# Performance work log

Measured on AMD Instinct MI355X. Metric: run time of the kernel, lower is better.

## Reference

```python
import jax, jax.numpy as jnp
import numpy as np

N, M, K = 100000, 50000, 8   # num vertices, num hyperedges, fixed hyperedge size
DIN, DOUT = 128, 128

def setup_inputs() -> dict:
    key = jax.random.key(0)
    k1, k2, k3 = jax.random.split(key, 3)
    X = jax.random.normal(k1, (N, DIN), jnp.float32)
    vertex = jax.random.randint(k2, (M * K,), 0, N)          # member vertices, flattened
    edges = jnp.repeat(jnp.arange(M), K)                     # hyperedge id per entry (sorted)
    W = jax.random.normal(k3, (DIN, DOUT), jnp.float32) / np.sqrt(DIN)
    b = jnp.zeros((DOUT,), jnp.float32)
    return {"X": X, "vertex": vertex, "edges": edges, "W": W, "b": b}

def reference(X, vertex, edges, W, b):
    # theta: Linear(in, out) applied BEFORE graph construction (as in dhg.HyperGCNConv)
    Y = X @ W + b                              # [N, DOUT]
    verts = vertex.reshape(M, K)               # hyperedge membership (edges = repeat(arange(M), K))
    feats = Y[verts]                           # [M, K, DOUT] gather
    # pairwise squared distances within each hyperedge
    sq = jnp.sum(feats * feats, axis=-1)                      # [M, K]
    d2 = sq[:, :, None] + sq[:, None, :] - 2.0 * jnp.einsum('mkd,mld->mkl', feats, feats)
    flat = jnp.argmax(d2.reshape(M, K * K), axis=1)
    ui, vi = flat // K, flat % K                              # argmax-distance pair positions
    u = jnp.take_along_axis(verts, ui[:, None], 1)[:, 0]      # [M]
    v = jnp.take_along_axis(verts, vi[:, None], 1)[:, 0]      # [M]
    w = jnp.float32(1.0 / (2 * K - 3))                        # HyperGCN mediator weight
    pos = jnp.arange(K)
    med = ((pos[None, :] != ui[:, None]) & (pos[None, :] != vi[:, None])).astype(Y.dtype)  # [M,K]
    # graph edges: (u,v) + (u,m),(v,m) for each mediator m; masked entries get weight 0
    src = jnp.concatenate([u, jnp.repeat(u, K), jnp.repeat(v, K)])
    dst = jnp.concatenate([v, verts.reshape(-1), verts.reshape(-1)])
    wts = jnp.concatenate([jnp.full((M,), w, Y.dtype), (med * w).reshape(-1), (med * w).reshape(-1)])
    # GCN smoothing: D^{-1/2} (A + I) D^{-1/2} Y with symmetric A, duplicate edges summed
    deg = jnp.ones((N,), Y.dtype).at[src].add(wts).at[dst].add(wts)
    dinv = jax.lax.rsqrt(deg)
    Xs = Y * dinv[:, None]
    out = Xs                                                  # self-loop term
    out = out.at[dst].add(wts[:, None] * Xs[src])
    out = out.at[src].add(wts[:, None] * Xs[dst])
    out = out * dinv[:, None]
    return jax.nn.relu(out)                                   # is_last=False -> ReLU (dropout=0)
```

## Files before the change

kernel.cpp:

```cpp
#include <hip/hip_runtime.h>
#include <hip/hip_bf16.h>

#define NV 100000
#define ME 50000
#define NINC (ME * 8)
#define NBLK ((NV + 255) / 256)
#define NRBG ((NV + 127) / 128)
constexpr float WMED = 1.0f / 13.0f;

typedef __attribute__((ext_vector_type(8))) short bf16x8;
typedef __attribute__((ext_vector_type(4))) float f32x4;

static __device__ inline void cvt_split8(const float4& a, const float4& b,
                                         bf16x8& hi, bf16x8& lo) {
    const float v[8] = {a.x, a.y, a.z, a.w, b.x, b.y, b.z, b.w};
    #pragma unroll
    for (int j = 0; j < 8; ++j) {
        __hip_bfloat16 h = __float2bfloat16(v[j]);
        const float hf = __bfloat162float(h);
        __hip_bfloat16 l = __float2bfloat16(v[j] - hf);
        union { __hip_bfloat16 b; short s; } uh{h}, ul{l};
        hi[j] = uh.s;
        lo[j] = ul.s;
    }
}

__global__ __launch_bounds__(256) void k_wsplit(const float* __restrict__ W,
                                                short* __restrict__ Wg) {
    const int idx = blockIdx.x * 256 + threadIdx.x;
    const int k = idx >> 7;
    const int c = idx & 127;
    const float w = W[idx];
    __hip_bfloat16 h = __float2bfloat16(w);
    const float hf = __bfloat162float(h);
    __hip_bfloat16 l = __float2bfloat16(w - hf);
    const int cb = c >> 6, gp = (c >> 4) & 3, m = c & 15;
    const int s = k >> 5, qq = (k >> 3) & 3, j = k & 7;
    const int base = cb * 1024 + (s * 4 + gp) * 64 + qq * 16 + m;
    union { __hip_bfloat16 b; short s; } uh{h}, ul{l};
    Wg[(long)base * 8 + j] = uh.s;
    Wg[(long)(2048 + base) * 8 + j] = ul.s;
}

__global__ __launch_bounds__(256, 4) void k_gemm(const float* __restrict__ X,
                                                 const uint4* __restrict__ Wg,
                                                 const float* __restrict__ bias,
                                                 float* __restrict__ Y,
                                                 __hip_bfloat16* __restrict__ Ybf) {
    const int t = threadIdx.x;
    const int wv = t >> 6;
    const int L  = t & 63;
    const int m  = L & 15;
    const int q  = L >> 4;

    const int rb = blockIdx.x >> 1;
    const int cb = blockIdx.x & 1;

    const int row_base = rb * 128 + wv * 32;
    int r0 = row_base + m;      if (r0 > NV - 1) r0 = NV - 1;
    int r1 = row_base + 16 + m; if (r1 > NV - 1) r1 = NV - 1;
    const float* p0 = X + (long)r0 * 128 + q * 8;
    const float* p1 = X + (long)r1 * 128 + q * 8;

    const bf16x8* Whf = (const bf16x8*)Wg + cb * 1024;
    const bf16x8* Wlf = (const bf16x8*)Wg + 2048 + cb * 1024;

    f32x4 acc[2][4];
    #pragma unroll
    for (int tt = 0; tt < 2; ++tt)
        #pragma unroll
        for (int g = 0; g < 4; ++g)
            acc[tt][g] = (f32x4){0.f, 0.f, 0.f, 0.f};

    float4 Ac0 = *(const float4*)(p0);
    float4 Ac1 = *(const float4*)(p0 + 4);
    float4 Ac2 = *(const float4*)(p1);
    float4 Ac3 = *(const float4*)(p1 + 4);

    #pragma unroll
    for (int s = 0; s < 4; ++s) {
        float4 An0, An1, An2, An3;
        if (s < 3) {
            An0 = *(const float4*)(p0 + (s + 1) * 32);
            An1 = *(const float4*)(p0 + (s + 1) * 32 + 4);
            An2 = *(const float4*)(p1 + (s + 1) * 32);
            An3 = *(const float4*)(p1 + (s + 1) * 32 + 4);
        }
        bf16x8 ah0, al0, ah1, al1;
        cvt_split8(Ac0, Ac1, ah0, al0);
        cvt_split8(Ac2, Ac3, ah1, al1);
        #pragma unroll
        for (int g = 0; g < 4; ++g) {
            const bf16x8 bh = Whf[(s * 4 + g) * 64 + L];
            const bf16x8 bl = Wlf[(s * 4 + g) * 64 + L];
            acc[0][g] = __builtin_amdgcn_mfma_f32_16x16x32_bf16(ah0, bh, acc[0][g], 0, 0, 0);
            acc[0][g] = __builtin_amdgcn_mfma_f32_16x16x32_bf16(ah0, bl, acc[0][g], 0, 0, 0);
            acc[0][g] = __builtin_amdgcn_mfma_f32_16x16x32_bf16(al0, bh, acc[0][g], 0, 0, 0);
            acc[1][g] = __builtin_amdgcn_mfma_f32_16x16x32_bf16(ah1, bh, acc[1][g], 0, 0, 0);
            acc[1][g] = __builtin_amdgcn_mfma_f32_16x16x32_bf16(ah1, bl, acc[1][g], 0, 0, 0);
            acc[1][g] = __builtin_amdgcn_mfma_f32_16x16x32_bf16(al1, bh, acc[1][g], 0, 0, 0);
        }
        if (s < 3) { Ac0 = An0; Ac1 = An1; Ac2 = An2; Ac3 = An3; }
    }

    float bc[4];
    #pragma unroll
    for (int g = 0; g < 4; ++g) bc[g] = bias[cb * 64 + g * 16 + m];

    #pragma unroll
    for (int tt = 0; tt < 2; ++tt) {
        #pragma unroll
        for (int r = 0; r < 4; ++r) {
            const int row = row_base + tt * 16 + q * 4 + r;
            float vg[4], vn[4];
            #pragma unroll
            for (int g = 0; g < 4; ++g) {
                vg[g] = acc[tt][g][r] + bc[g];
                vn[g] = __shfl_xor(vg[g], 1);
            }
            if (row < NV) {
                #pragma unroll
                for (int g = 0; g < 4; ++g)
                    Y[(long)row * 128 + cb * 64 + g * 16 + m] = vg[g];
                if ((L & 1) == 0) {
                    #pragma unroll
                    for (int g = 0; g < 4; ++g) {
                        __hip_bfloat162 h2;
                        h2.x = __float2bfloat16(vg[g]);
                        h2.y = __float2bfloat16(vn[g]);
                        *(__hip_bfloat162*)(Ybf + (long)row * 128 + cb * 64 + g * 16 + m) = h2;
                    }
                }
            }
        }
    }
}

__global__ __launch_bounds__(256) void k_edge(const float* __restrict__ Y,
                                              const int* __restrict__ vertex,
                                              int* __restrict__ uvpos) {
    const int wid = threadIdx.x >> 6;
    const int lane = threadIdx.x & 63;
    const int m = blockIdx.x * 4 + wid;

    const int x = lane & 15;
    const int q = lane >> 4;
    const int vr = vertex[m * 8 + (x & 7)];
    const float* rp = Y + (long)vr * 128 + q * 8;

    float4 A0[4], A1[4];
    #pragma unroll
    for (int s = 0; s < 4; ++s) {
        A0[s] = *(const float4*)(rp + s * 32);
        A1[s] = *(const float4*)(rp + s * 32 + 4);
    }

    f32x4 acc = (f32x4){0.f, 0.f, 0.f, 0.f};
    #pragma unroll
    for (int s = 0; s < 4; ++s) {
        bf16x8 ah, al;
        cvt_split8(A0[s], A1[s], ah, al);
        acc = __builtin_amdgcn_mfma_f32_16x16x32_bf16(ah, ah, acc, 0, 0, 0);
        acc = __builtin_amdgcn_mfma_f32_16x16x32_bf16(ah, al, acc, 0, 0, 0);
        acc = __builtin_amdgcn_mfma_f32_16x16x32_bf16(al, ah, acc, 0, 0, 0);
    }

    const int k = lane >> 3, l = lane & 7;
    const int srcG = l + 16 * (k >> 2);
    const int srcK = k + 16 * (k >> 2);
    const int srcL = l + 16 * (l >> 2);
    float g = 0.f, sk = 0.f, sl = 0.f;
    #pragma unroll
    for (int r = 0; r < 4; ++r) {
        const float tg = __shfl(acc[r], srcG);
        const float tk = __shfl(acc[r], srcK);
        const float tl = __shfl(acc[r], srcL);
        if ((k & 3) == r) { g = tg; sk = tk; }
        if ((l & 3) == r) sl = tl;
    }
    float v = sk + sl - 2.0f * g;

    int idx = lane;
    #pragma unroll
    for (int off = 32; off >= 1; off >>= 1) {
        const float ov = __shfl_xor(v, off);
        const int oi = __shfl_xor(idx, off);
        if (ov > v || (ov == v && oi < idx)) { v = ov; idx = oi; }
    }
    if (lane == 0) uvpos[m] = idx;
}

__global__ __launch_bounds__(256) void k_init(int* __restrict__ cnt,
                                              int* __restrict__ rowptr) {
    const int i = blockIdx.x * 256 + threadIdx.x;
    if (i < NV) cnt[i] = 0;
    if (i == 0) rowptr[NV] = NINC;
}

__global__ __launch_bounds__(256) void k_hist(const int* __restrict__ vertex,
                                              int* __restrict__ cnt) {
    const int j = blockIdx.x * 256 + threadIdx.x;
    if (j < NINC) atomicAdd(cnt + vertex[j], 1);
}

__global__ __launch_bounds__(256) void k_scan1(const int* __restrict__ cnt,
                                               int* __restrict__ bsum) {
    __shared__ int s[256];
    const int t = threadIdx.x;
    const int i = blockIdx.x * 256 + t;
    s[t] = (i < NV) ? cnt[i] : 0;
    __syncthreads();
    #pragma unroll
    for (int off = 128; off >= 1; off >>= 1) {
        if (t < off) s[t] += s[t + off];
        __syncthreads();
    }
    if (t == 0) bsum[blockIdx.x] = s[0];
}

__global__ __launch_bounds__(64) void k_scan2(const int* __restrict__ bsum,
                                              int* __restrict__ boff) {
    const int lane = threadIdx.x;
    int running = 0;
    for (int c = 0; c * 64 < NBLK; ++c) {
        const int idx = c * 64 + lane;
        int v = (idx < NBLK) ? bsum[idx] : 0;
        int x = v;
        #pragma unroll
        for (int off = 1; off < 64; off <<= 1) {
            const int n = __shfl_up(x, off);
            if (lane >= off) x += n;
        }
        if (idx < NBLK) boff[idx] = running + x - v;
        running += __shfl(x, 63);
    }
}

__global__ __launch_bounds__(256) void k_scan3(const int* __restrict__ cnt,
                                               const int* __restrict__ boff,
                                               int* __restrict__ rowptr,
                                               int* __restrict__ fill) {
    __shared__ int s[256];
    const int t = threadIdx.x;
    const int i = blockIdx.x * 256 + t;
    const int v = (i < NV) ? cnt[i] : 0;
    s[t] = v;
    __syncthreads();
    #pragma unroll
    for (int off = 1; off < 256; off <<= 1) {
        const int add = (t >= off) ? s[t - off] : 0;
        __syncthreads();
        s[t] += add;
        __syncthreads();
    }
    if (i < NV) {
        const int excl = boff[blockIdx.x] + s[t] - v;
        rowptr[i] = excl;
        fill[i] = excl;
    }
}

__global__ __launch_bounds__(256) void k_fill(const int* __restrict__ vertex,
                                              const int* __restrict__ uvpos,
                                              int* __restrict__ fill,
                                              int* __restrict__ entries) {
    const int j = blockIdx.x * 256 + threadIdx.x;
    if (j < NINC) {
        const int v = vertex[j];
        const int m = j >> 3, p = j & 7;
        const int idx = uvpos[m];
        const int role = (p == (idx >> 3) || p == (idx & 7)) ? 0 : 1;
        const int slot = atomicAdd(fill + v, 1);
        entries[slot] = (m << 1) | role;
    }
}

__global__ __launch_bounds__(256) void k_deg(const int* __restrict__ rowptr,
                                             const int* __restrict__ entries,
                                             float* __restrict__ deg) {
    const int i = blockIdx.x * 256 + threadIdx.x;
    if (i >= NV) return;
    const int start = rowptr[i], end = rowptr[i + 1];
    float d = 1.0f;
    for (int e = start; e < end; ++e)
        d += (entries[e] & 1) ? (2.0f * WMED) : (7.0f * WMED);
    deg[i] = d;
}

__global__ __launch_bounds__(256) void k_sp(const __hip_bfloat16* __restrict__ Ybf,
                                            const int* __restrict__ vertex,
                                            const int* __restrict__ uvpos,
                                            const float* __restrict__ deg,
                                            __hip_bfloat162* __restrict__ SP) {
    const int wid = threadIdx.x >> 6;
    const int lane = threadIdx.x & 63;
    const int m = blockIdx.x * 4 + wid;

    const int idx = uvpos[m];
    const int ui = idx >> 3, vi = idx & 7;

    float S0 = 0.f, S1 = 0.f, U0 = 0.f, U1 = 0.f, V0 = 0.f, V1 = 0.f;
    #pragma unroll
    for (int p = 0; p < 8; ++p) {
        const int vp = vertex[m * 8 + p];
        const float di = rsqrtf(deg[vp]);
        const __hip_bfloat162 y2 =
            ((const __hip_bfloat162*)(Ybf + (long)vp * 128))[lane];
        const float r0 = __bfloat162float(y2.x) * di;
        const float r1 = __bfloat162float(y2.y) * di;
        S0 += r0; S1 += r1;
        if (p == ui) { U0 = r0; U1 = r1; }
        if (p == vi) { V0 = r0; V1 = r1; }
    }
    __hip_bfloat162 s2, p2;
    s2.x = __float2bfloat16(WMED * S0);
    s2.y = __float2bfloat16(WMED * S1);
    p2.x = __float2bfloat16(WMED * (U0 + V0));
    p2.y = __float2bfloat16(WMED * (U1 + V1));
    SP[(long)(2 * m) * 64 + lane] = s2;
    SP[(long)(2 * m + 1) * 64 + lane] = p2;
}

__global__ __launch_bounds__(256) void k_gather(const float* __restrict__ Y,
                                                const float* __restrict__ deg,
                                                const int* __restrict__ rowptr,
                                                const int* __restrict__ entries,
                                                const __hip_bfloat162* __restrict__ SP,
                                                float* __restrict__ out) {
    const int wid = threadIdx.x >> 6;
    const int lane = threadIdx.x & 63;
    const int i = blockIdx.x * 4 + wid;

    const int start = rowptr[i], end = rowptr[i + 1];
    const int degc = end - start;
    const int tl = (lane < degc) ? entries[start + lane] : 0;

    const float din = rsqrtf(deg[i]);
    const float2 y = *(const float2*)(Y + (long)i * 128 + lane * 2);
    const float xs0 = y.x * din;
    const float xs1 = y.y * din;

    float a0 = 0.f, a1 = 0.f;
    float fnuv = 0.f;
    const int dmain = (degc < 64) ? degc : 64;

    for (int e = 0; e < dmain; e += 4) {
        const int j1 = (e + 1 < dmain) ? e + 1 : e;
        const int j2 = (e + 2 < dmain) ? e + 2 : e;
        const int j3 = (e + 3 < dmain) ? e + 3 : e;
        const float m1 = (e + 1 < dmain) ? 1.f : 0.f;
        const float m2 = (e + 2 < dmain) ? 1.f : 0.f;
        const float m3 = (e + 3 < dmain) ? 1.f : 0.f;
        const int t0 = __shfl(tl, e);
        const int t1 = __shfl(tl, j1);
        const int t2 = __shfl(tl, j2);
        const int t3 = __shfl(tl, j3);
        const __hip_bfloat162 T0 = SP[(long)t0 * 64 + lane];
        const __hip_bfloat162 T1 = SP[(long)t1 * 64 + lane];
        const __hip_bfloat162 T2 = SP[(long)t2 * 64 + lane];
        const __hip_bfloat162 T3 = SP[(long)t3 * 64 + lane];
        fnuv += (float)((t0 & 1) ^ 1) + m1 * (float)((t1 & 1) ^ 1)
              + m2 * (float)((t2 & 1) ^ 1) + m3 * (float)((t3 & 1) ^ 1);
        a0 += __bfloat162float(T0.x) + m1 * __bfloat162float(T1.x)
            + m2 * __bfloat162float(T2.x) + m3 * __bfloat162float(T3.x);
        a1 += __bfloat162float(T0.y) + m1 * __bfloat162float(T1.y)
            + m2 * __bfloat162float(T2.y) + m3 * __bfloat162float(T3.y);
    }
    for (int e2 = start + 64; e2 < end; ++e2) {
        const int t = entries[e2];
        const __hip_bfloat162 T = SP[(long)t * 64 + lane];
        fnuv += (float)((t & 1) ^ 1);
        a0 += __bfloat162float(T.x);
        a1 += __bfloat162float(T.y);
    }

    const float self = 1.0f - WMED * fnuv;
    a0 = fmaf(self, xs0, a0);
    a1 = fmaf(self, xs1, a1);
    float2 o;
    o.x = fmaxf(a0 * din, 0.0f);
    o.y = fmaxf(a1 * din, 0.0f);
    *(float2*)(out + (long)i * 128 + lane * 2) = o;
}

extern "C" void kernel_launch(void* const* d_in, const int* in_sizes, int n_in,
                              void* d_out, int out_size, void* d_ws, size_t ws_size,
                              hipStream_t stream) {
    const float* X      = (const float*)d_in[0];
    const int*   vertex = (const int*)d_in[1];
    const float* W      = (const float*)d_in[3];
    const float* bias   = (const float*)d_in[4];
    float* out = (float*)d_out;

    float* Y              = (float*)d_ws;
    __hip_bfloat16* Ybf   = (__hip_bfloat16*)(Y + (long)NV * 128);
    __hip_bfloat162* SP   = (__hip_bfloat162*)(Ybf + (long)NV * 128);
    float* deg            = (float*)((__hip_bfloat16*)SP + (long)2 * ME * 128);
    int*   uvpos          = (int*)(deg + NV);
    int*   cnt            = uvpos + ME;
    int*   rowptr         = cnt + NV;
    int*   fill           = rowptr + NV + 1;
    int*   bsum           = fill + NV;
    int*   boff           = bsum + NBLK;
    int*   entries        = boff + NBLK;
    char*  pW             = (char*)(entries + NINC);
    uint4* Wg             = (uint4*)(((uintptr_t)pW + 15) & ~(uintptr_t)15);

    k_wsplit<<<64, 256, 0, stream>>>(W, (short*)Wg);
    k_gemm <<<NRBG * 2, 256, 0, stream>>>(X, Wg, bias, Y, Ybf);
    k_edge <<<ME / 4, 256, 0, stream>>>(Y, vertex, uvpos);
    k_init <<<NBLK, 256, 0, stream>>>(cnt, rowptr);
    k_hist <<<(NINC + 255) / 256, 256, 0, stream>>>(vertex, cnt);
    k_scan1<<<NBLK, 256, 0, stream>>>(cnt, bsum);
    k_scan2<<<1, 64, 0, stream>>>(bsum, boff);
    k_scan3<<<NBLK, 256, 0, stream>>>(cnt, boff, rowptr, fill);
    k_fill <<<(NINC + 255) / 256, 256, 0, stream>>>(vertex, uvpos, fill, entries);
    k_deg  <<<NBLK, 256, 0, stream>>>(rowptr, entries, deg);
    k_sp   <<<ME / 4, 256, 0, stream>>>(Ybf, vertex, uvpos, deg, SP);
    k_gather<<<NV / 4, 256, 0, stream>>>(Y, deg, rowptr, entries, SP, out);
}
```

Baseline: 284.4 us.

## Compute edge distances with FP32 LDS dot products and fold degree into fill

The per-hyperedge pairwise distance kernel now stages the 8 member rows in shared memory and computes the 8x8 Gram matrix with FP32 FMAs, one pair per lane. This replaces the split-bf16 MFMA path and its shuffle gymnastics, and gives exact FP32 argmax. Separately, the degree computation kernel is removed: k_init sets deg to 1, and k_fill atomically adds each incidence's weight. This saves one launch and a CSR pass, at the cost of float atomics and a non-deterministic summation order.

```diff
diff --git a/kernel.cpp b/kernel.cpp
--- a/kernel.cpp
+++ b/kernel.cpp
@@ -139,47 +139,47 @@
 __global__ __launch_bounds__(256) void k_edge(const float* __restrict__ Y,
                                               const int* __restrict__ vertex,
                                               int* __restrict__ uvpos) {
+    __shared__ float sF[4][8 * 132];
     const int wid = threadIdx.x >> 6;
     const int lane = threadIdx.x & 63;
     const int m = blockIdx.x * 4 + wid;
-
-    const int x = lane & 15;
-    const int q = lane >> 4;
-    const int vr = vertex[m * 8 + (x & 7)];
-    const float* rp = Y + (long)vr * 128 + q * 8;
-
-    float4 A0[4], A1[4];
-    #pragma unroll
-    for (int s = 0; s < 4; ++s) {
-        A0[s] = *(const float4*)(rp + s * 32);
-        A1[s] = *(const float4*)(rp + s * 32 + 4);
-    }
-
-    f32x4 acc = (f32x4){0.f, 0.f, 0.f, 0.f};
-    #pragma unroll
-    for (int s = 0; s < 4; ++s) {
-        bf16x8 ah, al;
-        cvt_split8(A0[s], A1[s], ah, al);
-        acc = __builtin_amdgcn_mfma_f32_16x16x32_bf16(ah, ah, acc, 0, 0, 0);
-        acc = __builtin_amdgcn_mfma_f32_16x16x32_bf16(ah, al, acc, 0, 0, 0);
-        acc = __builtin_amdgcn_mfma_f32_16x16x32_bf16(al, ah, acc, 0, 0, 0);
-    }
+    float* F = sF[wid];
+
+    int verts[8];
+    #pragma unroll
+    for (int p = 0; p < 8; ++p) verts[p] = vertex[m * 8 + p];
+
+    #pragma unroll
+    for (int p = 0; p < 8; ++p) {
+        const float2 v = *(const float2*)(Y + (long)verts[p] * 128 + lane * 2);
+        *(float2*)(F + p * 132 + lane * 2) = v;
+    }
+    __syncthreads();
 
     const int k = lane >> 3, l = lane & 7;
-    const int srcG = l + 16 * (k >> 2);
-    const int srcK = k + 16 * (k >> 2);
-    const int srcL = l + 16 * (l >> 2);
-    float g = 0.f, sk = 0.f, sl = 0.f;
-    #pragma unroll
-    for (int r = 0; r < 4; ++r) {
-        const float tg = __shfl(acc[r], srcG);
-        const float tk = __shfl(acc[r], srcK);
-        const float tl = __shfl(acc[r], srcL);
-        if ((k & 3) == r) { g = tg; sk = tk; }
-        if ((l & 3) == r) sl = tl;
-    }
-    float v = sk + sl - 2.0f * g;
-
+    float a0 = 0.f, a1 = 0.f, a2 = 0.f, a3 = 0.f;
+    const float4* ra = (const float4*)(F + k * 132);
+    const float4* rb = (const float4*)(F + l * 132);
+    #pragma unroll
+    for (int d4 = 0; d4 < 32; d4 += 4) {
+        const float4 x0 = ra[d4],     y0 = rb[d4];
+        const float4 x1 = ra[d4 + 1], y1 = rb[d4 + 1];
+        const float4 x2 = ra[d4 + 2], y2 = rb[d4 + 2];
+        const float4 x3 = ra[d4 + 3], y3 = rb[d4 + 3];
+        a0 = fmaf(x0.x, y0.x, a0); a0 = fmaf(x0.y, y0.y, a0);
+        a0 = fmaf(x0.z, y0.z, a0); a0 = fmaf(x0.w, y0.w, a0);
+        a1 = fmaf(x1.x, y1.x, a1); a1 = fmaf(x1.y, y1.y, a1);
+        a1 = fmaf(x1.z, y1.z, a1); a1 = fmaf(x1.w, y1.w, a1);
+        a2 = fmaf(x2.x, y2.x, a2); a2 = fmaf(x2.y, y2.y, a2);
+        a2 = fmaf(x2.z, y2.z, a2); a2 = fmaf(x2.w, y2.w, a2);
+        a3 = fmaf(x3.x, y3.x, a3); a3 = fmaf(x3.y, y3.y, a3);
+        a3 = fmaf(x3.z, y3.z, a3); a3 = fmaf(x3.w, y3.w, a3);
+    }
+    const float acc = (a0 + a1) + (a2 + a3);
+
+    const float sqk = __shfl(acc, k * 9);
+    const float sql = __shfl(acc, l * 9);
+    float v = sqk + sql - 2.0f * acc;
     int idx = lane;
     #pragma unroll
     for (int off = 32; off >= 1; off >>= 1) {
@@ -191,9 +191,10 @@
 }
 
 __global__ __launch_bounds__(256) void k_init(int* __restrict__ cnt,
+                                              float* __restrict__ deg,
                                               int* __restrict__ rowptr) {
     const int i = blockIdx.x * 256 + threadIdx.x;
-    if (i < NV) cnt[i] = 0;
+    if (i < NV) { cnt[i] = 0; deg[i] = 1.0f; }
     if (i == 0) rowptr[NV] = NINC;
 }
 
@@ -263,7 +264,8 @@
 __global__ __launch_bounds__(256) void k_fill(const int* __restrict__ vertex,
                                               const int* __restrict__ uvpos,
                                               int* __restrict__ fill,
-                                              int* __restrict__ entries) {
+                                              int* __restrict__ entries,
+                                              float* __restrict__ deg) {
     const int j = blockIdx.x * 256 + threadIdx.x;
     if (j < NINC) {
         const int v = vertex[j];
@@ -272,19 +274,8 @@
         const int role = (p == (idx >> 3) || p == (idx & 7)) ? 0 : 1;
         const int slot = atomicAdd(fill + v, 1);
         entries[slot] = (m << 1) | role;
-    }
-}
-
-__global__ __launch_bounds__(256) void k_deg(const int* __restrict__ rowptr,
-                                             const int* __restrict__ entries,
-                                             float* __restrict__ deg) {
-    const int i = blockIdx.x * 256 + threadIdx.x;
-    if (i >= NV) return;
-    const int start = rowptr[i], end = rowptr[i + 1];
-    float d = 1.0f;
-    for (int e = start; e < end; ++e)
-        d += (entries[e] & 1) ? (2.0f * WMED) : (7.0f * WMED);
-    deg[i] = d;
+        atomicAdd(deg + v, role ? (2.0f * WMED) : (7.0f * WMED));
+    }
 }
 
 __global__ __launch_bounds__(256) void k_sp(const __hip_bfloat16* __restrict__ Ybf,
@@ -409,13 +400,12 @@
     k_wsplit<<<64, 256, 0, stream>>>(W, (short*)Wg);
     k_gemm <<<NRBG * 2, 256, 0, stream>>>(X, Wg, bias, Y, Ybf);
     k_edge <<<ME / 4, 256, 0, stream>>>(Y, vertex, uvpos);
-    k_init <<<NBLK, 256, 0, stream>>>(cnt, rowptr);
+    k_init <<<NBLK, 256, 0, stream>>>(cnt, deg, rowptr);
     k_hist <<<(NINC + 255) / 256, 256, 0, stream>>>(vertex, cnt);
     k_scan1<<<NBLK, 256, 0, stream>>>(cnt, bsum);
     k_scan2<<<1, 64, 0, stream>>>(bsum, boff);
     k_scan3<<<NBLK, 256, 0, stream>>>(cnt, boff, rowptr, fill);
-    k_fill <<<(NINC + 255) / 256, 256, 0, stream>>>(vertex, uvpos, fill, entries);
-    k_deg  <<<NBLK, 256, 0, stream>>>(rowptr, entries, deg);
+    k_fill <<<(NINC + 255) / 256, 256, 0, stream>>>(vertex, uvpos, fill, entries, deg);
     k_sp   <<<ME / 4, 256, 0, stream>>>(Ybf, vertex, uvpos, deg, SP);
     k_gather<<<NV / 4, 256, 0, stream>>>(Y, deg, rowptr, entries, SP, out);
 }
```

Result: slower. 295.8 us (+4.0%).
